# Performance work log

Measured on AMD Instinct MI355X. Metric: run time of the kernel, lower is better.

## Reference

```python
import jax, jax.numpy as jnp
import numpy as np

N_NODES = 50000
N_EDGES = 800000
IN_SIZE = 128
HIDDEN = 128   # out_size * 2
OUT_SIZE = 64


def setup_inputs() -> dict:
    key = jax.random.key(0)
    ks = jax.random.split(key, 6)
    h = jax.random.normal(ks[0], (N_NODES, IN_SIZE), dtype=jnp.float32)
    W1 = jax.random.normal(ks[1], (IN_SIZE, HIDDEN), dtype=jnp.float32) * (1.0 / np.sqrt(IN_SIZE))
    b1 = jnp.zeros((HIDDEN,), dtype=jnp.float32)
    W2 = jax.random.normal(ks[2], (HIDDEN, OUT_SIZE), dtype=jnp.float32) * (1.0 / np.sqrt(HIDDEN))
    b2 = jnp.zeros((OUT_SIZE,), dtype=jnp.float32)
    src = jax.random.randint(ks[3], (N_EDGES,), 0, N_NODES, dtype=jnp.int64)
    dst = jax.random.randint(ks[4], (N_EDGES,), 0, N_NODES, dtype=jnp.int64)
    return {"h": h, "W1": W1, "b1": b1, "W2": W2, "b2": b2, "src": src, "dst": dst}


def _norms(src, dst, n_nodes):
    # DGL GraphConv norm='both': scale by out_degree^{-1/2} (src side)
    # and in_degree^{-1/2} (dst side); zero degrees clamped to 1.
    ones = jnp.ones(src.shape, dtype=jnp.float32)
    out_deg = jnp.maximum(jax.ops.segment_sum(ones, src, num_segments=n_nodes), 1.0)
    in_deg = jnp.maximum(jax.ops.segment_sum(ones, dst, num_segments=n_nodes), 1.0)
    return (out_deg ** -0.5)[:, None], (in_deg ** -0.5)[:, None]


def _graph_conv(x, W, b, src, dst, norm_out, norm_in, n_nodes):
    # h' = D_in^{-1/2} A D_out^{-1/2} x W + b
    x = x * norm_out                                   # [N, F]
    agg = jax.ops.segment_sum(x[src], dst, num_segments=n_nodes)  # SpMM: [N, F]
    return (agg * norm_in) @ W + b


def reference(h, W1, b1, W2, b2, src, dst):
    n_nodes = h.shape[0]
    norm_out, norm_in = _norms(src, dst, n_nodes)
    h = jax.nn.relu(_graph_conv(h, W1, b1, src, dst, norm_out, norm_in, n_nodes))
    h = jax.nn.relu(_graph_conv(h, W2, b2, src, dst, norm_out, norm_in, n_nodes))
    return h
```

## Files before the change

kernel.cpp:

```cpp
#include <hip/hip_runtime.h>

#define N_NODES 50000
#define N_EDGES 800000
#define IN_SIZE 128
#define HIDDEN 128
#define OUT_SIZE 64

#define CHUNKS 128
#define CHUNK_EDGES 6250
#define GEMMA_TILES 1563
#define SCAN_BLK 1024
#define SCAN_GRID 49

static __device__ inline unsigned pack_bf16x2(float a, float b) {
    unsigned ua = __float_as_uint(a);
    unsigned ub = __float_as_uint(b);
    unsigned ra = (ua + 0x7fffu + ((ua >> 16) & 1u)) >> 16;
    unsigned rb = (ub + 0x7fffu + ((ub >> 16) & 1u)) & 0xffff0000u;
    return ra | rb;
}

__global__ __launch_bounds__(1024) void hist_kernel(const int* __restrict__ src,
                                                    const int* __restrict__ dst,
                                                    unsigned char* __restrict__ cntD,
                                                    unsigned char* __restrict__ cntS,
                                                    unsigned char* __restrict__ rp) {
    __shared__ unsigned hD[12500];
    __shared__ unsigned hS[12500];
    const int t = threadIdx.x;
    const int c = blockIdx.x;

    for (int i = t; i < 12500; i += 1024) { hD[i] = 0u; hS[i] = 0u; }
    __syncthreads();

    const int base = c * CHUNK_EDGES;
    for (int i = t; i < CHUNK_EDGES; i += 1024) {
        int e = base + i;
        int d = dst[e];
        int s = src[e];
        unsigned shd = (unsigned)(d & 3) * 8u;
        unsigned old = atomicAdd(&hD[d >> 2], 1u << shd);
        rp[e] = (unsigned char)((old >> shd) & 0xffu);
        atomicAdd(&hS[s >> 2], 1u << ((unsigned)(s & 3) * 8u));
    }
    __syncthreads();

    unsigned* gD = (unsigned*)cntD + (size_t)c * 12500;
    unsigned* gS = (unsigned*)cntS + (size_t)c * 12500;
    for (int i = t; i < 12500; i += 1024) { gD[i] = hD[i]; gS[i] = hS[i]; }
}

__global__ __launch_bounds__(256) void colscan_kernel(unsigned char* __restrict__ cntD,
                                                      const unsigned char* __restrict__ cntS,
                                                      int* __restrict__ deg_in,
                                                      float* __restrict__ norm_out,
                                                      float* __restrict__ norm_in) {
    int n = blockIdx.x * 256 + threadIdx.x;
    if (n >= N_NODES) return;
    unsigned sumD = 0u, sumS = 0u;
    #pragma unroll 4
    for (int c = 0; c < CHUNKS; ++c) {
        size_t idx = (size_t)c * 50000 + n;
        unsigned v = cntD[idx];
        cntD[idx] = (unsigned char)sumD;
        sumD += v;
        sumS += cntS[idx];
    }
    deg_in[n]   = (int)sumD;
    norm_in[n]  = rsqrtf((float)(sumD ? sumD : 1u));
    norm_out[n] = rsqrtf((float)(sumS ? sumS : 1u));
}

__global__ __launch_bounds__(256) void gemmA_kernel(const float* __restrict__ h,
                                                    const float* __restrict__ W1,
                                                    unsigned short* __restrict__ t1) {
    __shared__ float sA[32][128];
    __shared__ float sW[32][128];

    const int tile = blockIdx.x;
    const int t  = threadIdx.x;
    const int tx = t & 31;
    const int ty = t >> 5;
    const int n0 = tile * 32;

    for (int i = t; i < 1024; i += 256) {
        int n = i >> 5, c = i & 31;
        int gn = n0 + n;
        float4 v = make_float4(0.f, 0.f, 0.f, 0.f);
        if (gn < N_NODES) v = ((const float4*)(h + (size_t)gn * 128))[c];
        ((float4*)sA[n])[c] = v;
    }

    float4 acc[4];
    #pragma unroll
    for (int i = 0; i < 4; ++i) acc[i] = make_float4(0.f, 0.f, 0.f, 0.f);

    for (int kc = 0; kc < 4; ++kc) {
        __syncthreads();
        for (int i = t; i < 1024; i += 256) {
            int k = i >> 5, c = i & 31;
            ((float4*)sW[k])[c] = ((const float4*)(W1 + (size_t)(kc * 32 + k) * 128))[c];
        }
        __syncthreads();
        #pragma unroll 8
        for (int k = 0; k < 32; ++k) {
            float4 w = ((float4*)sW[k])[tx];
            #pragma unroll
            for (int ni = 0; ni < 4; ++ni) {
                float a = sA[ty * 4 + ni][kc * 32 + k];
                acc[ni].x = fmaf(a, w.x, acc[ni].x);
                acc[ni].y = fmaf(a, w.y, acc[ni].y);
                acc[ni].z = fmaf(a, w.z, acc[ni].z);
                acc[ni].w = fmaf(a, w.w, acc[ni].w);
            }
        }
    }

    #pragma unroll
    for (int ni = 0; ni < 4; ++ni) {
        int gn = n0 + ty * 4 + ni;
        if (gn < N_NODES) {
            uint2 p;
            p.x = pack_bf16x2(acc[ni].x, acc[ni].y);
            p.y = pack_bf16x2(acc[ni].z, acc[ni].w);
            ((uint2*)(t1 + (size_t)gn * 128))[tx] = p;
        }
    }
}

__global__ __launch_bounds__(SCAN_BLK) void scan1_kernel(const int* __restrict__ deg_in,
                                                         int* __restrict__ row_ptr,
                                                         int* __restrict__ bsum) {
    __shared__ int wsum[16];
    const int t = threadIdx.x, lane = t & 63, w = t >> 6;
    const int i = blockIdx.x * SCAN_BLK + t;
    int v = (i < N_NODES) ? deg_in[i] : 0;
    int incl = v;
    #pragma unroll
    for (int d = 1; d < 64; d <<= 1) {
        int u = __shfl_up(incl, d, 64);
        if (lane >= d) incl += u;
    }
    if (lane == 63) wsum[w] = incl;
    __syncthreads();
    int woff = 0, total = 0;
    #pragma unroll
    for (int j = 0; j < 16; ++j) {
        int s = wsum[j];
        if (j < w) woff += s;
        total += s;
    }
    if (i < N_NODES) row_ptr[i] = woff + incl - v;
    if (t == 0) bsum[blockIdx.x] = total;
}

__global__ __launch_bounds__(64) void scan2_kernel(int* __restrict__ bsum) {
    const int t = threadIdx.x;
    int v = (t < SCAN_GRID) ? bsum[t] : 0;
    int incl = v;
    #pragma unroll
    for (int d = 1; d < 64; d <<= 1) {
        int u = __shfl_up(incl, d, 64);
        if (t >= d) incl += u;
    }
    if (t < SCAN_GRID) bsum[t] = incl - v;
}

__global__ __launch_bounds__(SCAN_BLK) void scan3_kernel(int* __restrict__ row_ptr,
                                                         const int* __restrict__ bsum) {
    const int i = blockIdx.x * SCAN_BLK + threadIdx.x;
    if (i < N_NODES) row_ptr[i] += bsum[blockIdx.x];
    if (i == 0) row_ptr[N_NODES] = N_EDGES;
}

__global__ __launch_bounds__(256) void place_kernel(const int* __restrict__ src,
                                                    const int* __restrict__ dst,
                                                    const int* __restrict__ row_ptr,
                                                    const unsigned char* __restrict__ cntD,
                                                    const unsigned char* __restrict__ rp,
                                                    int* __restrict__ eidx) {
    int e = blockIdx.x * 256 + threadIdx.x;
    if (e < N_EDGES) {
        int d = dst[e];
        int c = e / CHUNK_EDGES;
        int pos = row_ptr[d] + (int)cntD[(size_t)c * 50000 + d] + (int)rp[e];
        eidx[pos] = src[e];
    }
}

__global__ __launch_bounds__(256) void gemmB_kernel(const float* __restrict__ h1p,
                                                    const float* __restrict__ W2,
                                                    float* __restrict__ t2) {
    __shared__ float sA[32][128];
    __shared__ float sW[128][64];
    const int t  = threadIdx.x;
    const int tx = t & 15;
    const int ty = t >> 4;
    const int n0 = blockIdx.x * 32;

    for (int i = t; i < 1024; i += 256) {
        int n = i >> 5, c = i & 31;
        int gn = n0 + n;
        float4 v = make_float4(0.f, 0.f, 0.f, 0.f);
        if (gn < N_NODES) v = ((const float4*)(h1p + (size_t)gn * 128))[c];
        ((float4*)sA[n])[c] = v;
    }
    for (int i = t; i < 2048; i += 256) {
        int k = i >> 4, c = i & 15;
        ((float4*)sW[k])[c] = ((const float4*)(W2 + (size_t)k * 64))[c];
    }
    __syncthreads();

    float4 a0 = make_float4(0.f, 0.f, 0.f, 0.f);
    float4 a1 = make_float4(0.f, 0.f, 0.f, 0.f);
    #pragma unroll 8
    for (int k = 0; k < 128; ++k) {
        float4 w = ((float4*)sW[k])[tx];
        float x0 = sA[ty * 2 + 0][k];
        float x1 = sA[ty * 2 + 1][k];
        a0.x = fmaf(x0, w.x, a0.x); a0.y = fmaf(x0, w.y, a0.y);
        a0.z = fmaf(x0, w.z, a0.z); a0.w = fmaf(x0, w.w, a0.w);
        a1.x = fmaf(x1, w.x, a1.x); a1.y = fmaf(x1, w.y, a1.y);
        a1.z = fmaf(x1, w.z, a1.z); a1.w = fmaf(x1, w.w, a1.w);
    }

    #pragma unroll
    for (int ni = 0; ni < 2; ++ni) {
        int gn = n0 + ty * 2 + ni;
        if (gn < N_NODES) ((float4*)(t2 + (size_t)gn * 64))[tx] = ni ? a1 : a0;
    }
}

__global__ __launch_bounds__(256) void pull128_kernel(const unsigned short* __restrict__ xb,
                                                      const int* __restrict__ row_ptr,
                                                      const int* __restrict__ eidx,
                                                      const float* __restrict__ b1,
                                                      const float* __restrict__ norm_in,
                                                      const float* __restrict__ norm_out,
                                                      float* __restrict__ out) {
    int node = blockIdx.x * 4 + (threadIdx.x >> 6);
    node = __builtin_amdgcn_readfirstlane(node);
    const int lane = threadIdx.x & 63;
    const int beg = __builtin_amdgcn_readfirstlane(row_ptr[node]);
    const int end = __builtin_amdgcn_readfirstlane(row_ptr[node + 1]);

    float2 acc0 = make_float2(0.f, 0.f);
    float2 acc1 = make_float2(0.f, 0.f);
    float2 acc2 = make_float2(0.f, 0.f);
    float2 acc3 = make_float2(0.f, 0.f);

    for (int base = beg; base < end; base += 64) {
        const int cnt = min(64, end - base);
        int my_e = 0;
        float my_n = 0.f;
        if (lane < cnt) {
            my_e = eidx[base + lane];
            my_n = norm_out[my_e];
        }
        int k = 0;
        for (; k + 3 < cnt; k += 4) {
            int s0 = __builtin_amdgcn_readlane(my_e, k);
            int s1 = __builtin_amdgcn_readlane(my_e, k + 1);
            int s2 = __builtin_amdgcn_readlane(my_e, k + 2);
            int s3 = __builtin_amdgcn_readlane(my_e, k + 3);
            float n0 = __int_as_float(__builtin_amdgcn_readlane(__float_as_int(my_n), k));
            float n1 = __int_as_float(__builtin_amdgcn_readlane(__float_as_int(my_n), k + 1));
            float n2 = __int_as_float(__builtin_amdgcn_readlane(__float_as_int(my_n), k + 2));
            float n3 = __int_as_float(__builtin_amdgcn_readlane(__float_as_int(my_n), k + 3));
            unsigned u0 = ((const unsigned*)(xb + (size_t)s0 * 128))[lane];
            unsigned u1 = ((const unsigned*)(xb + (size_t)s1 * 128))[lane];
            unsigned u2 = ((const unsigned*)(xb + (size_t)s2 * 128))[lane];
            unsigned u3 = ((const unsigned*)(xb + (size_t)s3 * 128))[lane];
            acc0.x = fmaf(__uint_as_float(u0 << 16), n0, acc0.x);
            acc0.y = fmaf(__uint_as_float(u0 & 0xffff0000u), n0, acc0.y);
            acc1.x = fmaf(__uint_as_float(u1 << 16), n1, acc1.x);
            acc1.y = fmaf(__uint_as_float(u1 & 0xffff0000u), n1, acc1.y);
            acc2.x = fmaf(__uint_as_float(u2 << 16), n2, acc2.x);
            acc2.y = fmaf(__uint_as_float(u2 & 0xffff0000u), n2, acc2.y);
            acc3.x = fmaf(__uint_as_float(u3 << 16), n3, acc3.x);
            acc3.y = fmaf(__uint_as_float(u3 & 0xffff0000u), n3, acc3.y);
        }
        for (; k < cnt; ++k) {
            int s0 = __builtin_amdgcn_readlane(my_e, k);
            float n0 = __int_as_float(__builtin_amdgcn_readlane(__float_as_int(my_n), k));
            unsigned u0 = ((const unsigned*)(xb + (size_t)s0 * 128))[lane];
            acc0.x = fmaf(__uint_as_float(u0 << 16), n0, acc0.x);
            acc0.y = fmaf(__uint_as_float(u0 & 0xffff0000u), n0, acc0.y);
        }
    }

    float ni = norm_in[node];
    float no = norm_out[node];
    float2 bb = ((const float2*)b1)[lane];
    float sx = (acc0.x + acc1.x) + (acc2.x + acc3.x);
    float sy = (acc0.y + acc1.y) + (acc2.y + acc3.y);
    float2 r;
    r.x = fmaxf(fmaf(sx, ni, bb.x), 0.f) * no;
    r.y = fmaxf(fmaf(sy, ni, bb.y), 0.f) * no;
    ((float2*)(out + (size_t)node * 128))[lane] = r;
}

__global__ __launch_bounds__(256) void pull64_kernel(const float* __restrict__ x,
                                                     const int* __restrict__ row_ptr,
                                                     const int* __restrict__ eidx,
                                                     const float* __restrict__ b2,
                                                     const float* __restrict__ norm_in,
                                                     float* __restrict__ out) {
    int node = blockIdx.x * 4 + (threadIdx.x >> 6);
    node = __builtin_amdgcn_readfirstlane(node);
    const int lane = threadIdx.x & 63;
    const int beg = __builtin_amdgcn_readfirstlane(row_ptr[node]);
    const int end = __builtin_amdgcn_readfirstlane(row_ptr[node + 1]);

    float a0 = 0.f, a1 = 0.f, a2 = 0.f, a3 = 0.f;
    for (int base = beg; base < end; base += 64) {
        const int cnt = min(64, end - base);
        int my_e = (lane < cnt) ? eidx[base + lane] : 0;
        int k = 0;
        for (; k + 3 < cnt; k += 4) {
            int s0 = __builtin_amdgcn_readlane(my_e, k);
            int s1 = __builtin_amdgcn_readlane(my_e, k + 1);
            int s2 = __builtin_amdgcn_readlane(my_e, k + 2);
            int s3 = __builtin_amdgcn_readlane(my_e, k + 3);
            a0 += x[(size_t)s0 * 64 + lane];
            a1 += x[(size_t)s1 * 64 + lane];
            a2 += x[(size_t)s2 * 64 + lane];
            a3 += x[(size_t)s3 * 64 + lane];
        }
        for (; k < cnt; ++k) {
            int s0 = __builtin_amdgcn_readlane(my_e, k);
            a0 += x[(size_t)s0 * 64 + lane];
        }
    }
    float ax = (a0 + a1) + (a2 + a3);
    float r = fmaxf(fmaf(ax, norm_in[node], b2[lane]), 0.f);
    out[(size_t)node * 64 + lane] = r;
}

extern "C" void kernel_launch(void* const* d_in, const int* in_sizes, int n_in,
                              void* d_out, int out_size, void* d_ws, size_t ws_size,
                              hipStream_t stream) {
    const float* h  = (const float*)d_in[0];
    const float* W1 = (const float*)d_in[1];
    const float* b1 = (const float*)d_in[2];
    const float* W2 = (const float*)d_in[3];
    const float* b2 = (const float*)d_in[4];
    const int* src  = (const int*)d_in[5];
    const int* dst  = (const int*)d_in[6];
    float* out = (float*)d_out;

    char* ws = (char*)d_ws;
    size_t off = 0;
    auto alloc = [&](size_t bytes) {
        void* p = ws + off;
        off = (off + bytes + 255) & ~(size_t)255;
        return p;
    };
    int* deg_in       = (int*)alloc(N_NODES * sizeof(int));
    float* norm_out   = (float*)alloc(N_NODES * sizeof(float));
    float* norm_in    = (float*)alloc(N_NODES * sizeof(float));
    int* row_ptr      = (int*)alloc((N_NODES + 1) * sizeof(int));
    int* bsum         = (int*)alloc(SCAN_GRID * sizeof(int));
    int* eidx         = (int*)alloc((size_t)N_EDGES * sizeof(int));
    unsigned short* t1 = (unsigned short*)alloc((size_t)N_NODES * 128 * sizeof(short));
    float* h1p        = (float*)alloc((size_t)N_NODES * 128 * sizeof(float));

    unsigned char* cntD = (unsigned char*)h1p;
    unsigned char* cntS = cntD + (size_t)CHUNKS * 50000;
    unsigned char* rp   = cntS + (size_t)CHUNKS * 50000;
    float* t2           = (float*)t1;

    hist_kernel<<<CHUNKS, 1024, 0, stream>>>(src, dst, cntD, cntS, rp);

    gemmA_kernel<<<GEMMA_TILES, 256, 0, stream>>>(h, W1, t1);

    colscan_kernel<<<(N_NODES + 255) / 256, 256, 0, stream>>>(cntD, cntS, deg_in,
                                                              norm_out, norm_in);

    scan1_kernel<<<SCAN_GRID, SCAN_BLK, 0, stream>>>(deg_in, row_ptr, bsum);
    scan2_kernel<<<1, 64, 0, stream>>>(bsum);
    scan3_kernel<<<SCAN_GRID, SCAN_BLK, 0, stream>>>(row_ptr, bsum);

    place_kernel<<<(N_EDGES + 255) / 256, 256, 0, stream>>>(src, dst, row_ptr, cntD, rp, eidx);

    pull128_kernel<<<N_NODES / 4, 256, 0, stream>>>(t1, row_ptr, eidx, b1, norm_in, norm_out, h1p);

    gemmB_kernel<<<(N_NODES + 31) / 32, 256, 0, stream>>>(h1p, W2, t2);
    pull64_kernel<<<N_NODES / 4, 256, 0, stream>>>(t2, row_ptr, eidx, b2, norm_in, out);
}
```

Measured before the change: 238.5 us.

## Fuse degree scan with block scan, store layer-2 features as fp16, widen gathers

The column-scan kernel now also does the per-block prefix scan. The third scan pass is dropped, and the block offset (bsum) is added lazily wherever row_ptr is read. The layer-2 intermediate t2 is stored as packed fp16 instead of fp32, which halves gather traffic in pull64. pull64 now has each half-wave handle a different edge, and pull128 gains an 8-way unrolled gather loop. This removes launches and memory traffic, at the cost of fp16 precision loss on t2 and extra bsum lookups in the pull kernels.

Measured after the change: 227.1 us. 4.8% less time.

```diff
diff --git a/kernel.cpp b/kernel.cpp
--- a/kernel.cpp
+++ b/kernel.cpp
@@ -9,8 +9,7 @@
 #define CHUNKS 128
 #define CHUNK_EDGES 6250
 #define GEMMA_TILES 1563
-#define SCAN_BLK 1024
-#define SCAN_GRID 49
+#define NBS 196
 
 static __device__ inline unsigned pack_bf16x2(float a, float b) {
     unsigned ua = __float_as_uint(a);
@@ -18,6 +17,19 @@
     unsigned ra = (ua + 0x7fffu + ((ua >> 16) & 1u)) >> 16;
     unsigned rb = (ub + 0x7fffu + ((ub >> 16) & 1u)) & 0xffff0000u;
     return ra | rb;
+}
+
+static __device__ inline unsigned pack_f16x2(float a, float b) {
+    _Float16 ha = (_Float16)a, hb = (_Float16)b;
+    unsigned short ua = __builtin_bit_cast(unsigned short, ha);
+    unsigned short ub = __builtin_bit_cast(unsigned short, hb);
+    return (unsigned)ua | ((unsigned)ub << 16);
+}
+
+static __device__ inline float2 unpack_f16x2(unsigned u) {
+    _Float16 lo = __builtin_bit_cast(_Float16, (unsigned short)(u & 0xffffu));
+    _Float16 hi = __builtin_bit_cast(_Float16, (unsigned short)(u >> 16));
+    return make_float2((float)lo, (float)hi);
 }
 
 __global__ __launch_bounds__(1024) void hist_kernel(const int* __restrict__ src,
@@ -50,25 +62,66 @@
     for (int i = t; i < 12500; i += 1024) { gD[i] = hD[i]; gS[i] = hS[i]; }
 }
 
-__global__ __launch_bounds__(256) void colscan_kernel(unsigned char* __restrict__ cntD,
-                                                      const unsigned char* __restrict__ cntS,
-                                                      int* __restrict__ deg_in,
-                                                      float* __restrict__ norm_out,
-                                                      float* __restrict__ norm_in) {
-    int n = blockIdx.x * 256 + threadIdx.x;
-    if (n >= N_NODES) return;
+__global__ __launch_bounds__(256) void deg_scan_kernel(unsigned char* __restrict__ cntD,
+                                                       const unsigned char* __restrict__ cntS,
+                                                       int* __restrict__ row_ptr,
+                                                       int* __restrict__ bsum,
+                                                       float* __restrict__ norm_out,
+                                                       float* __restrict__ norm_in) {
+    const int t = threadIdx.x, lane = t & 63, w = t >> 6;
+    const int n = blockIdx.x * 256 + t;
     unsigned sumD = 0u, sumS = 0u;
-    #pragma unroll 4
-    for (int c = 0; c < CHUNKS; ++c) {
-        size_t idx = (size_t)c * 50000 + n;
-        unsigned v = cntD[idx];
-        cntD[idx] = (unsigned char)sumD;
-        sumD += v;
-        sumS += cntS[idx];
-    }
-    deg_in[n]   = (int)sumD;
-    norm_in[n]  = rsqrtf((float)(sumD ? sumD : 1u));
-    norm_out[n] = rsqrtf((float)(sumS ? sumS : 1u));
+    if (n < N_NODES) {
+        #pragma unroll 4
+        for (int c = 0; c < CHUNKS; ++c) {
+            size_t idx = (size_t)c * 50000 + n;
+            unsigned v = cntD[idx];
+            cntD[idx] = (unsigned char)sumD;
+            sumD += v;
+            sumS += cntS[idx];
+        }
+        norm_in[n]  = rsqrtf((float)(sumD ? sumD : 1u));
+        norm_out[n] = rsqrtf((float)(sumS ? sumS : 1u));
+    }
+    __shared__ int wsum[4];
+    int v = (n < N_NODES) ? (int)sumD : 0;
+    int incl = v;
+    #pragma unroll
+    for (int d = 1; d < 64; d <<= 1) {
+        int u = __shfl_up(incl, d, 64);
+        if (lane >= d) incl += u;
+    }
+    if (lane == 63) wsum[w] = incl;
+    __syncthreads();
+    int woff = 0, total = 0;
+    #pragma unroll
+    for (int j = 0; j < 4; ++j) {
+        int s = wsum[j];
+        if (j < w) woff += s;
+        total += s;
+    }
+    if (n < N_NODES) row_ptr[n] = woff + incl - v;
+    if (t == 0) bsum[blockIdx.x] = total;
+}
+
+__global__ __launch_bounds__(64) void scan2_kernel(int* __restrict__ bsum,
+                                                   int* __restrict__ row_ptr) {
+    const int lane = threadIdx.x;
+    int carry = 0;
+    for (int base = 0; base < NBS; base += 64) {
+        int t = base + lane;
+        int v = (t < NBS) ? bsum[t] : 0;
+        int incl = v;
+        #pragma unroll
+        for (int d = 1; d < 64; d <<= 1) {
+            int u = __shfl_up(incl, d, 64);
+            if (lane >= d) incl += u;
+        }
+        int excl = carry + incl - v;
+        if (t < NBS) bsum[t] = excl;
+        if (t == NBS - 1) row_ptr[N_NODES] = N_EDGES - excl;
+        carry += __shfl(incl, 63, 64);
+    }
 }
 
 __global__ __launch_bounds__(256) void gemmA_kernel(const float* __restrict__ h,
@@ -128,54 +181,10 @@
     }
 }
 
-__global__ __launch_bounds__(SCAN_BLK) void scan1_kernel(const int* __restrict__ deg_in,
-                                                         int* __restrict__ row_ptr,
-                                                         int* __restrict__ bsum) {
-    __shared__ int wsum[16];
-    const int t = threadIdx.x, lane = t & 63, w = t >> 6;
-    const int i = blockIdx.x * SCAN_BLK + t;
-    int v = (i < N_NODES) ? deg_in[i] : 0;
-    int incl = v;
-    #pragma unroll
-    for (int d = 1; d < 64; d <<= 1) {
-        int u = __shfl_up(incl, d, 64);
-        if (lane >= d) incl += u;
-    }
-    if (lane == 63) wsum[w] = incl;
-    __syncthreads();
-    int woff = 0, total = 0;
-    #pragma unroll
-    for (int j = 0; j < 16; ++j) {
-        int s = wsum[j];
-        if (j < w) woff += s;
-        total += s;
-    }
-    if (i < N_NODES) row_ptr[i] = woff + incl - v;
-    if (t == 0) bsum[blockIdx.x] = total;
-}
-
-__global__ __launch_bounds__(64) void scan2_kernel(int* __restrict__ bsum) {
-    const int t = threadIdx.x;
-    int v = (t < SCAN_GRID) ? bsum[t] : 0;
-    int incl = v;
-    #pragma unroll
-    for (int d = 1; d < 64; d <<= 1) {
-        int u = __shfl_up(incl, d, 64);
-        if (t >= d) incl += u;
-    }
-    if (t < SCAN_GRID) bsum[t] = incl - v;
-}
-
-__global__ __launch_bounds__(SCAN_BLK) void scan3_kernel(int* __restrict__ row_ptr,
-                                                         const int* __restrict__ bsum) {
-    const int i = blockIdx.x * SCAN_BLK + threadIdx.x;
-    if (i < N_NODES) row_ptr[i] += bsum[blockIdx.x];
-    if (i == 0) row_ptr[N_NODES] = N_EDGES;
-}
-
 __global__ __launch_bounds__(256) void place_kernel(const int* __restrict__ src,
                                                     const int* __restrict__ dst,
                                                     const int* __restrict__ row_ptr,
+                                                    const int* __restrict__ bsum,
                                                     const unsigned char* __restrict__ cntD,
                                                     const unsigned char* __restrict__ rp,
                                                     int* __restrict__ eidx) {
@@ -183,14 +192,14 @@
     if (e < N_EDGES) {
         int d = dst[e];
         int c = e / CHUNK_EDGES;
-        int pos = row_ptr[d] + (int)cntD[(size_t)c * 50000 + d] + (int)rp[e];
+        int pos = row_ptr[d] + bsum[d >> 8] + (int)cntD[(size_t)c * 50000 + d] + (int)rp[e];
         eidx[pos] = src[e];
     }
 }
 
 __global__ __launch_bounds__(256) void gemmB_kernel(const float* __restrict__ h1p,
                                                     const float* __restrict__ W2,
-                                                    float* __restrict__ t2) {
+                                                    unsigned short* __restrict__ t2h) {
     __shared__ float sA[32][128];
     __shared__ float sW[128][64];
     const int t  = threadIdx.x;
@@ -227,12 +236,19 @@
     #pragma unroll
     for (int ni = 0; ni < 2; ++ni) {
         int gn = n0 + ty * 2 + ni;
-        if (gn < N_NODES) ((float4*)(t2 + (size_t)gn * 64))[tx] = ni ? a1 : a0;
+        if (gn < N_NODES) {
+            float4 a = ni ? a1 : a0;
+            uint2 p;
+            p.x = pack_f16x2(a.x, a.y);
+            p.y = pack_f16x2(a.z, a.w);
+            ((uint2*)(t2h + (size_t)gn * 64))[tx] = p;
+        }
     }
 }
 
 __global__ __launch_bounds__(256) void pull128_kernel(const unsigned short* __restrict__ xb,
                                                       const int* __restrict__ row_ptr,
+                                                      const int* __restrict__ bsum,
                                                       const int* __restrict__ eidx,
                                                       const float* __restrict__ b1,
                                                       const float* __restrict__ norm_in,
@@ -241,8 +257,8 @@
     int node = blockIdx.x * 4 + (threadIdx.x >> 6);
     node = __builtin_amdgcn_readfirstlane(node);
     const int lane = threadIdx.x & 63;
-    const int beg = __builtin_amdgcn_readfirstlane(row_ptr[node]);
-    const int end = __builtin_amdgcn_readfirstlane(row_ptr[node + 1]);
+    const int beg = __builtin_amdgcn_readfirstlane(row_ptr[node] + bsum[node >> 8]);
+    const int end = __builtin_amdgcn_readfirstlane(row_ptr[node + 1] + bsum[(node + 1) >> 8]);
 
     float2 acc0 = make_float2(0.f, 0.f);
     float2 acc1 = make_float2(0.f, 0.f);
@@ -258,6 +274,48 @@
             my_n = norm_out[my_e];
         }
         int k = 0;
+        for (; k + 7 < cnt; k += 8) {
+            int s0 = __builtin_amdgcn_readlane(my_e, k);
+            int s1 = __builtin_amdgcn_readlane(my_e, k + 1);
+            int s2 = __builtin_amdgcn_readlane(my_e, k + 2);
+            int s3 = __builtin_amdgcn_readlane(my_e, k + 3);
+            int s4 = __builtin_amdgcn_readlane(my_e, k + 4);
+            int s5 = __builtin_amdgcn_readlane(my_e, k + 5);
+            int s6 = __builtin_amdgcn_readlane(my_e, k + 6);
+            int s7 = __builtin_amdgcn_readlane(my_e, k + 7);
+            float n0 = __int_as_float(__builtin_amdgcn_readlane(__float_as_int(my_n), k));
+            float n1 = __int_as_float(__builtin_amdgcn_readlane(__float_as_int(my_n), k + 1));
+            float n2 = __int_as_float(__builtin_amdgcn_readlane(__float_as_int(my_n), k + 2));
+            float n3 = __int_as_float(__builtin_amdgcn_readlane(__float_as_int(my_n), k + 3));
+            float n4 = __int_as_float(__builtin_amdgcn_readlane(__float_as_int(my_n), k + 4));
+            float n5 = __int_as_float(__builtin_amdgcn_readlane(__float_as_int(my_n), k + 5));
+            float n6 = __int_as_float(__builtin_amdgcn_readlane(__float_as_int(my_n), k + 6));
+            float n7 = __int_as_float(__builtin_amdgcn_readlane(__float_as_int(my_n), k + 7));
+            unsigned u0 = ((const unsigned*)(xb + (size_t)s0 * 128))[lane];
+            unsigned u1 = ((const unsigned*)(xb + (size_t)s1 * 128))[lane];
+            unsigned u2 = ((const unsigned*)(xb + (size_t)s2 * 128))[lane];
+            unsigned u3 = ((const unsigned*)(xb + (size_t)s3 * 128))[lane];
+            unsigned u4 = ((const unsigned*)(xb + (size_t)s4 * 128))[lane];
+            unsigned u5 = ((const unsigned*)(xb + (size_t)s5 * 128))[lane];
+            unsigned u6 = ((const unsigned*)(xb + (size_t)s6 * 128))[lane];
+            unsigned u7 = ((const unsigned*)(xb + (size_t)s7 * 128))[lane];
+            acc0.x = fmaf(__uint_as_float(u0 << 16), n0, acc0.x);
+            acc0.y = fmaf(__uint_as_float(u0 & 0xffff0000u), n0, acc0.y);
+            acc1.x = fmaf(__uint_as_float(u1 << 16), n1, acc1.x);
+            acc1.y = fmaf(__uint_as_float(u1 & 0xffff0000u), n1, acc1.y);
+            acc2.x = fmaf(__uint_as_float(u2 << 16), n2, acc2.x);
+            acc2.y = fmaf(__uint_as_float(u2 & 0xffff0000u), n2, acc2.y);
+            acc3.x = fmaf(__uint_as_float(u3 << 16), n3, acc3.x);
+            acc3.y = fmaf(__uint_as_float(u3 & 0xffff0000u), n3, acc3.y);
+            acc0.x = fmaf(__uint_as_float(u4 << 16), n4, acc0.x);
+            acc0.y = fmaf(__uint_as_float(u4 & 0xffff0000u), n4, acc0.y);
+            acc1.x = fmaf(__uint_as_float(u5 << 16), n5, acc1.x);
+            acc1.y = fmaf(__uint_as_float(u5 & 0xffff0000u), n5, acc1.y);
+            acc2.x = fmaf(__uint_as_float(u6 << 16), n6, acc2.x);
+            acc2.y = fmaf(__uint_as_float(u6 & 0xffff0000u), n6, acc2.y);
+            acc3.x = fmaf(__uint_as_float(u7 << 16), n7, acc3.x);
+            acc3.y = fmaf(__uint_as_float(u7 & 0xffff0000u), n7, acc3.y);
+        }
         for (; k + 3 < cnt; k += 4) {
             int s0 = __builtin_amdgcn_readlane(my_e, k);
             int s1 = __builtin_amdgcn_readlane(my_e, k + 1);
@@ -300,8 +358,9 @@
     ((float2*)(out + (size_t)node * 128))[lane] = r;
 }
 
-__global__ __launch_bounds__(256) void pull64_kernel(const float* __restrict__ x,
+__global__ __launch_bounds__(256) void pull64_kernel(const unsigned* __restrict__ x,
                                                      const int* __restrict__ row_ptr,
+                                                     const int* __restrict__ bsum,
                                                      const int* __restrict__ eidx,
                                                      const float* __restrict__ b2,
                                                      const float* __restrict__ norm_in,
@@ -309,32 +368,76 @@
     int node = blockIdx.x * 4 + (threadIdx.x >> 6);
     node = __builtin_amdgcn_readfirstlane(node);
     const int lane = threadIdx.x & 63;
-    const int beg = __builtin_amdgcn_readfirstlane(row_ptr[node]);
-    const int end = __builtin_amdgcn_readfirstlane(row_ptr[node + 1]);
-
-    float a0 = 0.f, a1 = 0.f, a2 = 0.f, a3 = 0.f;
+    const int half = lane >> 5;
+    const int fl = lane & 31;
+    const int beg = __builtin_amdgcn_readfirstlane(row_ptr[node] + bsum[node >> 8]);
+    const int end = __builtin_amdgcn_readfirstlane(row_ptr[node + 1] + bsum[(node + 1) >> 8]);
+
+    float2 a0 = make_float2(0.f, 0.f);
+    float2 a1 = make_float2(0.f, 0.f);
+    float2 a2 = make_float2(0.f, 0.f);
+    float2 a3 = make_float2(0.f, 0.f);
+
     for (int base = beg; base < end; base += 64) {
         const int cnt = min(64, end - base);
         int my_e = (lane < cnt) ? eidx[base + lane] : 0;
         int k = 0;
-        for (; k + 3 < cnt; k += 4) {
-            int s0 = __builtin_amdgcn_readlane(my_e, k);
-            int s1 = __builtin_amdgcn_readlane(my_e, k + 1);
-            int s2 = __builtin_amdgcn_readlane(my_e, k + 2);
-            int s3 = __builtin_amdgcn_readlane(my_e, k + 3);
-            a0 += x[(size_t)s0 * 64 + lane];
-            a1 += x[(size_t)s1 * 64 + lane];
-            a2 += x[(size_t)s2 * 64 + lane];
-            a3 += x[(size_t)s3 * 64 + lane];
-        }
-        for (; k < cnt; ++k) {
-            int s0 = __builtin_amdgcn_readlane(my_e, k);
-            a0 += x[(size_t)s0 * 64 + lane];
-        }
-    }
-    float ax = (a0 + a1) + (a2 + a3);
-    float r = fmaxf(fmaf(ax, norm_in[node], b2[lane]), 0.f);
-    out[(size_t)node * 64 + lane] = r;
+        for (; k + 7 < cnt; k += 8) {
+            int sa0 = __builtin_amdgcn_readlane(my_e, k);
+            int sb0 = __builtin_amdgcn_readlane(my_e, k + 1);
+            int sa1 = __builtin_amdgcn_readlane(my_e, k + 2);
+            int sb1 = __builtin_amdgcn_readlane(my_e, k + 3);
+            int sa2 = __builtin_amdgcn_readlane(my_e, k + 4);
+            int sb2 = __builtin_amdgcn_readlane(my_e, k + 5);
+            int sa3 = __builtin_amdgcn_readlane(my_e, k + 6);
+            int sb3 = __builtin_amdgcn_readlane(my_e, k + 7);
+            int e0 = half ? sb0 : sa0;
+            int e1 = half ? sb1 : sa1;
+            int e2 = half ? sb2 : sa2;
+            int e3 = half ? sb3 : sa3;
+            unsigned u0 = x[(size_t)e0 * 32 + fl];
+            unsigned u1 = x[(size_t)e1 * 32 + fl];
+            unsigned u2 = x[(size_t)e2 * 32 + fl];
+            unsigned u3 = x[(size_t)e3 * 32 + fl];
+            float2 v0 = unpack_f16x2(u0);
+            float2 v1 = unpack_f16x2(u1);
+            float2 v2 = unpack_f16x2(u2);
+            float2 v3 = unpack_f16x2(u3);
+            a0.x += v0.x; a0.y += v0.y;
+            a1.x += v1.x; a1.y += v1.y;
+            a2.x += v2.x; a2.y += v2.y;
+            a3.x += v3.x; a3.y += v3.y;
+        }
+        for (; k + 1 < cnt; k += 2) {
+            int sa = __builtin_amdgcn_readlane(my_e, k);
+            int sb = __builtin_amdgcn_readlane(my_e, k + 1);
+            int e0 = half ? sb : sa;
+            unsigned u = x[(size_t)e0 * 32 + fl];
+            float2 v = unpack_f16x2(u);
+            a0.x += v.x; a0.y += v.y;
+        }
+        if (k < cnt) {
+            int sa = __builtin_amdgcn_readlane(my_e, k);
+            if (half == 0) {
+                unsigned u = x[(size_t)sa * 32 + fl];
+                float2 v = unpack_f16x2(u);
+                a0.x += v.x; a0.y += v.y;
+            }
+        }
+    }
+
+    float ax = (a0.x + a1.x) + (a2.x + a3.x);
+    float ay = (a0.y + a1.y) + (a2.y + a3.y);
+    ax += __shfl_xor(ax, 32, 64);
+    ay += __shfl_xor(ay, 32, 64);
+    if (half == 0) {
+        float ni = norm_in[node];
+        float2 bb = ((const float2*)b2)[fl];
+        float2 r;
+        r.x = fmaxf(fmaf(ax, ni, bb.x), 0.f);
+        r.y = fmaxf(fmaf(ay, ni, bb.y), 0.f);
+        ((float2*)(out + (size_t)node * 64))[fl] = r;
+    }
 }
 
 extern "C" void kernel_launch(void* const* d_in, const int* in_sizes, int n_in,
@@ -356,11 +459,10 @@
         off = (off + bytes + 255) & ~(size_t)255;
         return p;
     };
-    int* deg_in       = (int*)alloc(N_NODES * sizeof(int));
     float* norm_out   = (float*)alloc(N_NODES * sizeof(float));
     float* norm_in    = (float*)alloc(N_NODES * sizeof(float));
     int* row_ptr      = (int*)alloc((N_NODES + 1) * sizeof(int));
-    int* bsum         = (int*)alloc(SCAN_GRID * sizeof(int));
+    int* bsum         = (int*)alloc(NBS * sizeof(int));
     int* eidx         = (int*)alloc((size_t)N_EDGES * sizeof(int));
     unsigned short* t1 = (unsigned short*)alloc((size_t)N_NODES * 128 * sizeof(short));
     float* h1p        = (float*)alloc((size_t)N_NODES * 128 * sizeof(float));
@@ -368,23 +470,22 @@
     unsigned char* cntD = (unsigned char*)h1p;
     unsigned char* cntS = cntD + (size_t)CHUNKS * 50000;
     unsigned char* rp   = cntS + (size_t)CHUNKS * 50000;
-    float* t2           = (float*)t1;
+    unsigned short* t2h = t1;
 
     hist_kernel<<<CHUNKS, 1024, 0, stream>>>(src, dst, cntD, cntS, rp);
 
     gemmA_kernel<<<GEMMA_TILES, 256, 0, stream>>>(h, W1, t1);
 
-    colscan_kernel<<<(N_NODES + 255) / 256, 256, 0, stream>>>(cntD, cntS, deg_in,
-                                                              norm_out, norm_in);
-
-    scan1_kernel<<<SCAN_GRID, SCAN_BLK, 0, stream>>>(deg_in, row_ptr, bsum);
-    scan2_kernel<<<1, 64, 0, stream>>>(bsum);
-    scan3_kernel<<<SCAN_GRID, SCAN_BLK, 0, stream>>>(row_ptr, bsum);
-
-    place_kernel<<<(N_EDGES + 255) / 256, 256, 0, stream>>>(src, dst, row_ptr, cntD, rp, eidx);
-
-    pull128_kernel<<<N_NODES / 4, 256, 0, stream>>>(t1, row_ptr, eidx, b1, norm_in, norm_out, h1p);
-
-    gemmB_kernel<<<(N_NODES + 31) / 32, 256, 0, stream>>>(h1p, W2, t2);
-    pull64_kernel<<<N_NODES / 4, 256, 0, stream>>>(t2, row_ptr, eidx, b2, norm_in, out);
-}
+    deg_scan_kernel<<<NBS, 256, 0, stream>>>(cntD, cntS, row_ptr, bsum, norm_out, norm_in);
+
+    scan2_kernel<<<1, 64, 0, stream>>>(bsum, row_ptr);
+
+    place_kernel<<<(N_EDGES + 255) / 256, 256, 0, stream>>>(src, dst, row_ptr, bsum, cntD, rp, eidx);
+
+    pull128_kernel<<<N_NODES / 4, 256, 0, stream>>>(t1, row_ptr, bsum, eidx, b1,
+                                                    norm_in, norm_out, h1p);
+
+    gemmB_kernel<<<(N_NODES + 31) / 32, 256, 0, stream>>>(h1p, W2, t2h);
+    pull64_kernel<<<N_NODES / 4, 256, 0, stream>>>((const unsigned*)t2h, row_ptr, bsum, eidx,
+                                                   b2, norm_in, out);
+}
```
